# Performance work log

Measured on AMD Instinct MI355X. Metric: run time of the kernel, lower is better.

The kernel has to match this reference:

```python
import jax, jax.numpy as jnp
import numpy as np


def gcn_conv(x, edge_index, edge_weight, W, b):
    """PyG GCNConv: add self-loops (weight 1), symmetric degree norm, aggregate, linear."""
    N = x.shape[0]
    loop = jnp.arange(N, dtype=edge_index.dtype)
    src = jnp.concatenate([edge_index[0], loop])
    dst = jnp.concatenate([edge_index[1], loop])
    ew = jnp.concatenate([edge_weight, jnp.ones((N,), dtype=x.dtype)])
    deg = jax.ops.segment_sum(ew, dst, num_segments=N)
    dinv = jnp.where(deg > 0, jax.lax.rsqrt(deg), 0.0)
    norm = dinv[src] * ew * dinv[dst]            # [E+N]
    h = x @ W                                    # [N, out] transform first
    msg = h[src] * norm[:, None]                 # gather + scale
    out = jax.ops.segment_sum(msg, dst, num_segments=N)  # scatter-add
    return out + b


def l2norm(x, eps=1e-12):
    n = jnp.sqrt(jnp.sum(x * x, axis=-1, keepdims=True))
    return x / jnp.maximum(n, eps)


def setup_inputs() -> dict:
    key = jax.random.key(0)
    ks = jax.random.split(key, 16)
    N_net, E_net, N_dag, E_dag = 100000, 600000, 50000, 400000
    D_net, D_dag, H_net, H_dag = 128, 128, 128, 128
    s = lambda fan_in: 1.0 / np.sqrt(fan_in)
    return {
        "net_feat": jax.random.normal(ks[0], (N_net, D_net), jnp.float32),
        "net_edge_index": jax.random.randint(ks[1], (2, E_net), 0, N_net, jnp.int32),
        "net_edge_weights": jax.random.uniform(ks[2], (E_net,), jnp.float32),
        "dag_feat": jax.random.normal(ks[3], (N_dag, D_dag), jnp.float32),
        "dag_edge_index": jax.random.randint(ks[4], (2, E_dag), 0, N_dag, jnp.int32),
        "dag_edge_weights": jax.random.uniform(ks[5], (E_dag,), jnp.float32),
        "W_net": jax.random.normal(ks[6], (D_net, H_net), jnp.float32) * s(D_net),
        "b_net": jnp.zeros((H_net,), jnp.float32),
        "W_dag": jax.random.normal(ks[7], (D_dag, H_dag), jnp.float32) * s(D_dag),
        "b_dag": jnp.zeros((H_dag,), jnp.float32),
        "W1": jax.random.normal(ks[8], (H_net + H_dag, 64), jnp.float32) * s(H_net + H_dag),
        "b1": jnp.zeros((64,), jnp.float32),
        "W2": jax.random.normal(ks[9], (64, 1), jnp.float32) * s(64),
        "b2": jnp.zeros((1,), jnp.float32),
    }


def reference(net_feat, net_edge_index, net_edge_weights,
              dag_feat, dag_edge_index, dag_edge_weights,
              W_net, b_net, W_dag, b_dag, W1, b1, W2, b2):
    net_emb = jax.nn.relu(gcn_conv(net_feat, net_edge_index, net_edge_weights, W_net, b_net))
    dag_emb = jax.nn.relu(gcn_conv(dag_feat, dag_edge_index, dag_edge_weights, W_dag, b_dag))
    # normalize == True
    net_emb = l2norm(net_emb)
    dag_emb = l2norm(dag_emb)
    # net_batch/dag_batch are None: mean over nodes -> single state value
    net_vec = net_emb.mean(axis=0)
    dag_vec = dag_emb.mean(axis=0)
    combined = jnp.concatenate([net_vec, dag_vec], axis=-1)
    h = jax.nn.relu(combined @ W1 + b1)
    state_val = h @ W2 + b2
    return state_val
```

## Files before the change

### kernel.cpp

```cpp
#include <hip/hip_runtime.h>

#define FD 128
#define PAD 48
#define WSCALE 16777216.0f
#define WINV   5.9604645e-8f

typedef __attribute__((ext_vector_type(8))) short short8;
typedef __attribute__((ext_vector_type(4))) float f32x4;

__device__ inline unsigned short f2bf(float f) {
    unsigned u = __float_as_uint(f);
    return (unsigned short)((u + 0x7fffu + ((u >> 16) & 1u)) >> 16);
}
__device__ inline void bf4_to_f32(uint2 u, float& a, float& b, float& c, float& d) {
    a = __uint_as_float(u.x << 16);
    b = __uint_as_float(u.x & 0xffff0000u);
    c = __uint_as_float(u.y << 16);
    d = __uint_as_float(u.y & 0xffff0000u);
}
__device__ inline float pc_to_dinv(unsigned long long pv) {
    return rsqrtf((float)(pv & 0xffffffffull) * WINV + 1.0f);
}
__device__ inline void split1(float x, unsigned short& h, unsigned short& l) {
    unsigned u = __float_as_uint(x);
    unsigned hh = (u + 0x7fffu + ((u >> 16) & 1u)) >> 16;
    float r = x - __uint_as_float(hh << 16);
    unsigned u2 = __float_as_uint(r);
    h = (unsigned short)hh;
    l = (unsigned short)((u2 + 0x7fffu + ((u2 >> 16) & 1u)) >> 16);
}

__global__ __launch_bounds__(256) void bucket_pack(
        const int* __restrict__ ei_n, const float* __restrict__ ew_n,
        unsigned long long* __restrict__ pc_n, int2* __restrict__ el_n,
        int E_n, int GBn,
        const int* __restrict__ ei_d, const float* __restrict__ ew_d,
        unsigned long long* __restrict__ pc_d, int2* __restrict__ el_d,
        int E_d,
        const float* __restrict__ Wn, const float* __restrict__ Wd,
        unsigned short* __restrict__ Wpack) {
    int b = blockIdx.x;
    int packStart = (int)gridDim.x - 16;
    if (b >= packStart) {
        int p = b - packStart;
        int graph = p >> 3, pb = p & 7;
        const float* W = graph ? Wd : Wn;
        int c  = threadIdx.x & 127;
        int hh = threadIdx.x >> 7;
        int k0 = pb * 16 + hh * 8;
        short8 hv, lv;
        #pragma unroll
        for (int j = 0; j < 8; j++) {
            unsigned short hq, lq;
            split1(W[(k0 + j) * FD + c], hq, lq);
            hv[j] = (short)hq; lv[j] = (short)lq;
        }
        char* dst = (char*)Wpack + graph * 65536
                  + c * 256 + 16 * ((k0 >> 3) ^ (c & 15));
        *(short8*)dst = hv;
        *(short8*)(dst + 32768) = lv;
        return;
    }
    const int* ei; const float* ew; unsigned long long* pc; int2* el; int E, e;
    if (b < GBn) { ei = ei_n; ew = ew_n; pc = pc_n; el = el_n; E = E_n;
                   e = b * 256 + threadIdx.x; }
    else         { ei = ei_d; ew = ew_d; pc = pc_d; el = el_d; E = E_d;
                   e = (b - GBn) * 256 + threadIdx.x; }
    if (e < E) {
        int src = ei[e];
        int dst = ei[E + e];
        float w = ew[e];
        unsigned long long val =
            (1ull << 32) |
            (unsigned long long)(unsigned int)__float2uint_rn(w * WSCALE);
        unsigned long long old = atomicAdd(&pc[dst], val);
        unsigned int pos = (unsigned int)(old >> 32);
        if (pos < PAD)
            el[(size_t)dst * PAD + pos] = make_int2(src, __float_as_int(w));
    }
}

__global__ __launch_bounds__(256) void gemm_mfma(
        const float* __restrict__ X_n, const unsigned long long* __restrict__ pc_n,
        unsigned short* __restrict__ hs_n, int N_n, int Gn,
        const float* __restrict__ X_d, const unsigned long long* __restrict__ pc_d,
        unsigned short* __restrict__ hs_d, int N_d,
        const unsigned short* __restrict__ Wpack) {
    __shared__ unsigned short WL[2][128][128];

    const float* X; const unsigned long long* pc; unsigned short* hs; int N, r0;
    const char* wsrc;
    if (blockIdx.x < Gn) { X = X_n; pc = pc_n; hs = hs_n; N = N_n;
                           r0 = blockIdx.x * 128; wsrc = (const char*)Wpack; }
    else                 { X = X_d; pc = pc_d; hs = hs_d; N = N_d;
                           r0 = (blockIdx.x - Gn) * 128;
                           wsrc = (const char*)Wpack + 65536; }

    const int tid  = threadIdx.x;
    const int w    = tid >> 6;
    const int lane = tid & 63;
    const int c15  = lane & 15;
    const int g    = lane >> 4;

    {
        const float4* s4 = (const float4*)wsrc;
        float4* d4 = (float4*)WL;
        #pragma unroll
        for (int i = 0; i < 16; i++) d4[tid + i * 256] = s4[tid + i * 256];
    }
    __syncthreads();

    f32x4 acc[2][8] = {};

    const int row0 = r0 + 32 * w + c15;
    const float* x0p = X + (size_t)row0 * FD;
    const float* x1p = x0p + 16 * FD;
    const bool v0 = row0 < N, v1 = (row0 + 16) < N;

    #pragma unroll
    for (int kt = 0; kt < 4; kt++) {
        const int ko = 32 * kt + 8 * g;
        float4 a0 = {}, a1 = {}, c0 = {}, c1 = {};
        if (v0) { a0 = *(const float4*)(x0p + ko); c0 = *(const float4*)(x0p + ko + 4); }
        if (v1) { a1 = *(const float4*)(x1p + ko); c1 = *(const float4*)(x1p + ko + 4); }
        short8 ah0, al0, ah1, al1;
        {
            float xx[8] = {a0.x, a0.y, a0.z, a0.w, c0.x, c0.y, c0.z, c0.w};
            #pragma unroll
            for (int j = 0; j < 8; j++) {
                unsigned short hq, lq; split1(xx[j], hq, lq);
                ah0[j] = (short)hq; al0[j] = (short)lq;
            }
        }
        {
            float xx[8] = {a1.x, a1.y, a1.z, a1.w, c1.x, c1.y, c1.z, c1.w};
            #pragma unroll
            for (int j = 0; j < 8; j++) {
                unsigned short hq, lq; split1(xx[j], hq, lq);
                ah1[j] = (short)hq; al1[j] = (short)lq;
            }
        }

        const char* bbase = (const char*)WL + c15 * 256
                          + 16 * (((unsigned)(g + 4 * kt)) ^ (unsigned)c15);
        #pragma unroll
        for (int cf = 0; cf < 8; cf++) {
            short8 bh = *(const short8*)(bbase + cf * 4096);
            short8 bl = *(const short8*)(bbase + cf * 4096 + 32768);
            acc[0][cf] = __builtin_amdgcn_mfma_f32_16x16x32_bf16(ah0, bh, acc[0][cf], 0, 0, 0);
            acc[1][cf] = __builtin_amdgcn_mfma_f32_16x16x32_bf16(ah1, bh, acc[1][cf], 0, 0, 0);
            acc[0][cf] = __builtin_amdgcn_mfma_f32_16x16x32_bf16(al0, bh, acc[0][cf], 0, 0, 0);
            acc[1][cf] = __builtin_amdgcn_mfma_f32_16x16x32_bf16(al1, bh, acc[1][cf], 0, 0, 0);
            acc[0][cf] = __builtin_amdgcn_mfma_f32_16x16x32_bf16(ah0, bl, acc[0][cf], 0, 0, 0);
            acc[1][cf] = __builtin_amdgcn_mfma_f32_16x16x32_bf16(ah1, bl, acc[1][cf], 0, 0, 0);
        }
    }

    __syncthreads();
    unsigned short* OT = (unsigned short*)WL;
    #pragma unroll
    for (int rf = 0; rf < 2; rf++) {
        float dv[4];
        #pragma unroll
        for (int r = 0; r < 4; r++) {
            int row = r0 + 32 * w + 16 * rf + 4 * g + r;
            dv[r] = pc_to_dinv(row < N ? pc[row] : 0ull);
        }
        #pragma unroll
        for (int cf = 0; cf < 8; cf++) {
            #pragma unroll
            for (int r = 0; r < 4; r++) {
                int lrow = 32 * w + 16 * rf + 4 * g + r;
                unsigned byteo = (unsigned)(lrow * 256)
                               + (unsigned)((32 * cf + 2 * c15) ^ ((lrow & 15) << 4));
                *(unsigned short*)((char*)OT + byteo) = f2bf(acc[rf][cf][r] * dv[r]);
            }
        }
    }
    __syncthreads();
    #pragma unroll
    for (int p = 0; p < 8; p++) {
        int idx  = p * 256 + tid;
        int lrow = idx >> 4, ch = idx & 15;
        int row  = r0 + lrow;
        if (row < N) {
            uint4 v = *(const uint4*)((const char*)WL + lrow * 256
                                      + 16 * (ch ^ (lrow & 15)));
            *(uint4*)&hs[(size_t)row * FD + ch * 8] = v;
        }
    }
}

__global__ __launch_bounds__(256) void gather_reduce_both(
        const unsigned short* __restrict__ hs_n,
        const unsigned long long* __restrict__ pc_n, const int2* __restrict__ el_n,
        const float* __restrict__ b_n, int N_n,
        const unsigned short* __restrict__ hs_d,
        const unsigned long long* __restrict__ pc_d, const int2* __restrict__ el_d,
        const float* __restrict__ b_d, int N_d,
        float* __restrict__ vec) {
    __shared__ float accw[8][2 * FD];
    const int tid  = threadIdx.x;
    const int hw   = tid >> 5;
    const int sl   = tid & 31;

    float4 bbn = *(const float4*)&b_n[sl * 4];
    float4 bbd = *(const float4*)&b_d[sl * 4];
    float an0 = 0.f, an1 = 0.f, an2 = 0.f, an3 = 0.f;
    float ad0 = 0.f, ad1 = 0.f, ad2 = 0.f, ad3 = 0.f;

    const int total = N_n + N_d;
    const int stride = gridDim.x * 8;
    for (int t = blockIdx.x * 8 + hw; t < total; t += stride) {
        const bool isn = t < N_n;
        const int i = isn ? t : t - N_n;
        const unsigned short* hs = isn ? hs_n : hs_d;
        const unsigned long long* pc = isn ? pc_n : pc_d;
        const int2* el = (isn ? el_n : el_d) + (size_t)i * PAD;

        unsigned long long pv = pc[i];
        int cnt = (int)(pv >> 32);
        if (cnt > PAD) cnt = PAD;
        float dv = pc_to_dinv(pv);

        int2 my = (sl < cnt) ? el[sl] : make_int2(0, 0);

        float s0, s1, s2, s3;
        bf4_to_f32(*(const uint2*)&hs[(size_t)i * FD + sl * 4], s0, s1, s2, s3);
        float x0 = s0 * dv, x1 = s1 * dv, x2 = s2 * dv, x3 = s3 * dv;

        int lim = cnt < 32 ? cnt : 32;
        int j = 0;
        for (; j + 4 <= lim; j += 4) {
            int   q0 = __shfl(my.x, j,     32);
            float w0 = __int_as_float(__shfl(my.y, j,     32)) * dv;
            int   q1 = __shfl(my.x, j + 1, 32);
            float w1 = __int_as_float(__shfl(my.y, j + 1, 32)) * dv;
            int   q2 = __shfl(my.x, j + 2, 32);
            float w2 = __int_as_float(__shfl(my.y, j + 2, 32)) * dv;
            int   q3 = __shfl(my.x, j + 3, 32);
            float w3 = __int_as_float(__shfl(my.y, j + 3, 32)) * dv;
            uint2 u0 = *(const uint2*)&hs[(size_t)q0 * FD + sl * 4];
            uint2 u1 = *(const uint2*)&hs[(size_t)q1 * FD + sl * 4];
            uint2 u2 = *(const uint2*)&hs[(size_t)q2 * FD + sl * 4];
            uint2 u3 = *(const uint2*)&hs[(size_t)q3 * FD + sl * 4];
            float a, b2, c, d;
            bf4_to_f32(u0, a, b2, c, d);
            x0 = fmaf(a, w0, x0); x1 = fmaf(b2, w0, x1);
            x2 = fmaf(c, w0, x2); x3 = fmaf(d, w0, x3);
            bf4_to_f32(u1, a, b2, c, d);
            x0 = fmaf(a, w1, x0); x1 = fmaf(b2, w1, x1);
            x2 = fmaf(c, w1, x2); x3 = fmaf(d, w1, x3);
            bf4_to_f32(u2, a, b2, c, d);
            x0 = fmaf(a, w2, x0); x1 = fmaf(b2, w2, x1);
            x2 = fmaf(c, w2, x2); x3 = fmaf(d, w2, x3);
            bf4_to_f32(u3, a, b2, c, d);
            x0 = fmaf(a, w3, x0); x1 = fmaf(b2, w3, x1);
            x2 = fmaf(c, w3, x2); x3 = fmaf(d, w3, x3);
        }
        for (; j < lim; j++) {
            int   q = __shfl(my.x, j, 32);
            float w = __int_as_float(__shfl(my.y, j, 32)) * dv;
            uint2 u = *(const uint2*)&hs[(size_t)q * FD + sl * 4];
            float a, b2, c, d;
            bf4_to_f32(u, a, b2, c, d);
            x0 = fmaf(a, w, x0); x1 = fmaf(b2, w, x1);
            x2 = fmaf(c, w, x2); x3 = fmaf(d, w, x3);
        }
        for (; j < cnt; j++) {
            int2 p = el[j];
            float w = __int_as_float(p.y) * dv;
            uint2 u = *(const uint2*)&hs[(size_t)p.x * FD + sl * 4];
            float a, b2, c, d;
            bf4_to_f32(u, a, b2, c, d);
            x0 = fmaf(a, w, x0); x1 = fmaf(b2, w, x1);
            x2 = fmaf(c, w, x2); x3 = fmaf(d, w, x3);
        }

        float4 bb = isn ? bbn : bbd;
        x0 = fmaxf(x0 + bb.x, 0.f);
        x1 = fmaxf(x1 + bb.y, 0.f);
        x2 = fmaxf(x2 + bb.z, 0.f);
        x3 = fmaxf(x3 + bb.w, 0.f);
        float ss = fmaf(x0, x0, fmaf(x1, x1, fmaf(x2, x2, x3 * x3)));
        #pragma unroll
        for (int o = 16; o; o >>= 1) ss += __shfl_xor(ss, o);
        float inv = 1.0f / fmaxf(sqrtf(ss), 1e-12f);
        if (isn) {
            an0 = fmaf(x0, inv, an0); an1 = fmaf(x1, inv, an1);
            an2 = fmaf(x2, inv, an2); an3 = fmaf(x3, inv, an3);
        } else {
            ad0 = fmaf(x0, inv, ad0); ad1 = fmaf(x1, inv, ad1);
            ad2 = fmaf(x2, inv, ad2); ad3 = fmaf(x3, inv, ad3);
        }
    }
    accw[hw][sl * 4 + 0] = an0;
    accw[hw][sl * 4 + 1] = an1;
    accw[hw][sl * 4 + 2] = an2;
    accw[hw][sl * 4 + 3] = an3;
    accw[hw][FD + sl * 4 + 0] = ad0;
    accw[hw][FD + sl * 4 + 1] = ad1;
    accw[hw][FD + sl * 4 + 2] = ad2;
    accw[hw][FD + sl * 4 + 3] = ad3;
    __syncthreads();
    {
        float s = accw[0][tid] + accw[1][tid] + accw[2][tid] + accw[3][tid]
                + accw[4][tid] + accw[5][tid] + accw[6][tid] + accw[7][tid];
        unsafeAtomicAdd(&vec[tid], s);
    }
}

__global__ __launch_bounds__(256) void final_kernel(
        const float* __restrict__ vec,
        const float* __restrict__ W1, const float* __restrict__ b1,
        const float* __restrict__ W2, const float* __restrict__ b2,
        float* __restrict__ out, float invNnet, float invNdag) {
    __shared__ float part[4][64];
    int j = threadIdx.x & 63;
    int q = threadIdx.x >> 6;
    float h = 0.f;
    for (int k = q * 64; k < q * 64 + 64; k++) {
        float sc = (k < 128) ? invNnet : invNdag;
        h = fmaf(vec[k] * sc, W1[k * 64 + j], h);
    }
    part[q][j] = h;
    __syncthreads();
    if (threadIdx.x < 64) {
        float hh = b1[j] + part[0][j] + part[1][j] + part[2][j] + part[3][j];
        hh = fmaxf(hh, 0.f);
        float p = hh * W2[j];
        #pragma unroll
        for (int o = 32; o; o >>= 1) p += __shfl_xor(p, o);
        if (j == 0) out[0] = p + b2[0];
    }
}

extern "C" void kernel_launch(void* const* d_in, const int* in_sizes, int n_in,
                              void* d_out, int out_size, void* d_ws, size_t ws_size,
                              hipStream_t stream) {
    const float* net_feat = (const float*)d_in[0];
    const int*   net_ei   = (const int*)d_in[1];
    const float* net_ew   = (const float*)d_in[2];
    const float* dag_feat = (const float*)d_in[3];
    const int*   dag_ei   = (const int*)d_in[4];
    const float* dag_ew   = (const float*)d_in[5];
    const float* W_net    = (const float*)d_in[6];
    const float* b_net    = (const float*)d_in[7];
    const float* W_dag    = (const float*)d_in[8];
    const float* b_dag    = (const float*)d_in[9];
    const float* W1       = (const float*)d_in[10];
    const float* b1       = (const float*)d_in[11];
    const float* W2       = (const float*)d_in[12];
    const float* b2       = (const float*)d_in[13];

    const int N_net = in_sizes[0] / FD;
    const int E_net = in_sizes[2];
    const int N_dag = in_sizes[3] / FD;
    const int E_dag = in_sizes[5];
    const int GBn = (E_net + 255) / 256, GBd = (E_dag + 255) / 256;
    const int Gn  = (N_net + 127) / 128, Gd  = (N_dag + 127) / 128;

    char* w = (char*)d_ws;
    size_t o = 0;
    unsigned short* hs_net = (unsigned short*)(w + o); o += (size_t)2 * N_net * FD;
    unsigned short* hs_dag = (unsigned short*)(w + o); o += (size_t)2 * N_dag * FD;
    unsigned long long* pc_net = (unsigned long long*)(w + o); o += (size_t)8 * N_net;
    unsigned long long* pc_dag = (unsigned long long*)(w + o); o += (size_t)8 * N_dag;
    float* vec = (float*)(w + o); o += 256 * 4;
    size_t zbytes = (size_t)8 * (N_net + N_dag) + 256 * 4;
    int2* elist_net = (int2*)(w + o); o += (size_t)8 * N_net * PAD;
    int2* elist_dag = (int2*)(w + o); o += (size_t)8 * N_dag * PAD;
    unsigned short* Wpack = (unsigned short*)(w + o); o += 131072;

    hipMemsetAsync(pc_net, 0, zbytes, stream);

    bucket_pack<<<GBn + GBd + 16, 256, 0, stream>>>(
        net_ei, net_ew, pc_net, elist_net, E_net, GBn,
        dag_ei, dag_ew, pc_dag, elist_dag, E_dag,
        W_net, W_dag, Wpack);

    gemm_mfma<<<Gn + Gd, 256, 0, stream>>>(
        net_feat, pc_net, hs_net, N_net, Gn,
        dag_feat, pc_dag, hs_dag, N_dag, Wpack);

    gather_reduce_both<<<2048, 256, 0, stream>>>(
        hs_net, pc_net, elist_net, b_net, N_net,
        hs_dag, pc_dag, elist_dag, b_dag, N_dag, vec);

    final_kernel<<<1, 256, 0, stream>>>(vec, W1, b1, W2, b2, (float*)d_out,
                                        1.0f / (float)N_net, 1.0f / (float)N_dag);
}
```

Baseline: 346.7 us.

## Prefetch next node's metadata and batch neighbor gathers in groups of eight

After: 329.5 us. -5.0%, faster.

```diff
diff --git a/kernel.cpp b/kernel.cpp
--- a/kernel.cpp
+++ b/kernel.cpp
@@ -209,89 +209,139 @@
     float an0 = 0.f, an1 = 0.f, an2 = 0.f, an3 = 0.f;
     float ad0 = 0.f, ad1 = 0.f, ad2 = 0.f, ad3 = 0.f;
 
-    const int total = N_n + N_d;
+    const int total  = N_n + N_d;
     const int stride = gridDim.x * 8;
-    for (int t = blockIdx.x * 8 + hw; t < total; t += stride) {
-        const bool isn = t < N_n;
-        const int i = isn ? t : t - N_n;
-        const unsigned short* hs = isn ? hs_n : hs_d;
-        const unsigned long long* pc = isn ? pc_n : pc_d;
-        const int2* el = (isn ? el_n : el_d) + (size_t)i * PAD;
-
-        unsigned long long pv = pc[i];
-        int cnt = (int)(pv >> 32);
-        if (cnt > PAD) cnt = PAD;
-        float dv = pc_to_dinv(pv);
-
-        int2 my = (sl < cnt) ? el[sl] : make_int2(0, 0);
-
-        float s0, s1, s2, s3;
-        bf4_to_f32(*(const uint2*)&hs[(size_t)i * FD + sl * 4], s0, s1, s2, s3);
-        float x0 = s0 * dv, x1 = s1 * dv, x2 = s2 * dv, x3 = s3 * dv;
-
-        int lim = cnt < 32 ? cnt : 32;
-        int j = 0;
-        for (; j + 4 <= lim; j += 4) {
-            int   q0 = __shfl(my.x, j,     32);
-            float w0 = __int_as_float(__shfl(my.y, j,     32)) * dv;
-            int   q1 = __shfl(my.x, j + 1, 32);
-            float w1 = __int_as_float(__shfl(my.y, j + 1, 32)) * dv;
-            int   q2 = __shfl(my.x, j + 2, 32);
-            float w2 = __int_as_float(__shfl(my.y, j + 2, 32)) * dv;
-            int   q3 = __shfl(my.x, j + 3, 32);
-            float w3 = __int_as_float(__shfl(my.y, j + 3, 32)) * dv;
-            uint2 u0 = *(const uint2*)&hs[(size_t)q0 * FD + sl * 4];
-            uint2 u1 = *(const uint2*)&hs[(size_t)q1 * FD + sl * 4];
-            uint2 u2 = *(const uint2*)&hs[(size_t)q2 * FD + sl * 4];
-            uint2 u3 = *(const uint2*)&hs[(size_t)q3 * FD + sl * 4];
-            float a, b2, c, d;
-            bf4_to_f32(u0, a, b2, c, d);
-            x0 = fmaf(a, w0, x0); x1 = fmaf(b2, w0, x1);
-            x2 = fmaf(c, w0, x2); x3 = fmaf(d, w0, x3);
-            bf4_to_f32(u1, a, b2, c, d);
-            x0 = fmaf(a, w1, x0); x1 = fmaf(b2, w1, x1);
-            x2 = fmaf(c, w1, x2); x3 = fmaf(d, w1, x3);
-            bf4_to_f32(u2, a, b2, c, d);
-            x0 = fmaf(a, w2, x0); x1 = fmaf(b2, w2, x1);
-            x2 = fmaf(c, w2, x2); x3 = fmaf(d, w2, x3);
-            bf4_to_f32(u3, a, b2, c, d);
-            x0 = fmaf(a, w3, x0); x1 = fmaf(b2, w3, x1);
-            x2 = fmaf(c, w3, x2); x3 = fmaf(d, w3, x3);
-        }
-        for (; j < lim; j++) {
-            int   q = __shfl(my.x, j, 32);
-            float w = __int_as_float(__shfl(my.y, j, 32)) * dv;
-            uint2 u = *(const uint2*)&hs[(size_t)q * FD + sl * 4];
-            float a, b2, c, d;
-            bf4_to_f32(u, a, b2, c, d);
-            x0 = fmaf(a, w, x0); x1 = fmaf(b2, w, x1);
-            x2 = fmaf(c, w, x2); x3 = fmaf(d, w, x3);
-        }
-        for (; j < cnt; j++) {
-            int2 p = el[j];
-            float w = __int_as_float(p.y) * dv;
-            uint2 u = *(const uint2*)&hs[(size_t)p.x * FD + sl * 4];
-            float a, b2, c, d;
-            bf4_to_f32(u, a, b2, c, d);
-            x0 = fmaf(a, w, x0); x1 = fmaf(b2, w, x1);
-            x2 = fmaf(c, w, x2); x3 = fmaf(d, w, x3);
-        }
-
-        float4 bb = isn ? bbn : bbd;
-        x0 = fmaxf(x0 + bb.x, 0.f);
-        x1 = fmaxf(x1 + bb.y, 0.f);
-        x2 = fmaxf(x2 + bb.z, 0.f);
-        x3 = fmaxf(x3 + bb.w, 0.f);
-        float ss = fmaf(x0, x0, fmaf(x1, x1, fmaf(x2, x2, x3 * x3)));
-        #pragma unroll
-        for (int o = 16; o; o >>= 1) ss += __shfl_xor(ss, o);
-        float inv = 1.0f / fmaxf(sqrtf(ss), 1e-12f);
-        if (isn) {
-            an0 = fmaf(x0, inv, an0); an1 = fmaf(x1, inv, an1);
-            an2 = fmaf(x2, inv, an2); an3 = fmaf(x3, inv, an3);
-        } else {
-            ad0 = fmaf(x0, inv, ad0); ad1 = fmaf(x1, inv, ad1);
-            ad2 = fmaf(x2, inv, ad2); ad3 = fmaf(x3, inv, ad3);
+    int t0 = blockIdx.x * 8 + hw;
+
+    unsigned long long pvP = 0; int2 myP = make_int2(0, 0);
+    uint2 selfP = make_uint2(0u, 0u);
+
+    if (t0 < total) {
+        {
+            bool isn = t0 < N_n;
+            int i = isn ? t0 : t0 - N_n;
+            pvP   = (isn ? pc_n : pc_d)[i];
+            myP   = (isn ? el_n : el_d)[(size_t)i * PAD + sl];
+            selfP = *(const uint2*)&(isn ? hs_n : hs_d)[(size_t)i * FD + sl * 4];
+        }
+        for (int t = t0; t < total; t += stride) {
+            const unsigned long long pv = pvP;
+            const int2  my    = myP;
+            const uint2 selfu = selfP;
+            const bool isn = t < N_n;
+            const int  i   = isn ? t : t - N_n;
+            const unsigned short* hs = isn ? hs_n : hs_d;
+
+            int tn = t + stride;
+            if (tn < total) {
+                bool isn2 = tn < N_n;
+                int i2 = isn2 ? tn : tn - N_n;
+                pvP   = (isn2 ? pc_n : pc_d)[i2];
+                myP   = (isn2 ? el_n : el_d)[(size_t)i2 * PAD + sl];
+                selfP = *(const uint2*)&(isn2 ? hs_n : hs_d)[(size_t)i2 * FD + sl * 4];
+            }
+
+            int cnt = (int)(pv >> 32);
+            if (cnt > PAD) cnt = PAD;
+            const float dv = pc_to_dinv(pv);
+            const int lim = cnt < 32 ? cnt : 32;
+
+            float s0, s1, s2, s3;
+            bf4_to_f32(selfu, s0, s1, s2, s3);
+            float x0 = s0 * dv, x1 = s1 * dv, x2 = s2 * dv, x3 = s3 * dv;
+
+            uint2 ua[8]; float wa[8];
+            #pragma unroll
+            for (int u = 0; u < 8; u++) {
+                int   q  = __shfl(my.x, u, 32);
+                int   wi = __shfl(my.y, u, 32);
+                bool act = u < cnt;
+                wa[u] = act ? __int_as_float(wi) : 0.f;
+                int  qq = act ? q : i;
+                ua[u] = *(const uint2*)&hs[(size_t)qq * FD + sl * 4];
+            }
+            if (lim > 8) {
+                uint2 ub[8]; float wb[8];
+                #pragma unroll
+                for (int u = 0; u < 8; u++) {
+                    int  jj = 8 + u;
+                    int   q  = __shfl(my.x, jj, 32);
+                    int   wi = __shfl(my.y, jj, 32);
+                    bool act = jj < cnt;
+                    wb[u] = act ? __int_as_float(wi) : 0.f;
+                    int  qq = act ? q : i;
+                    ub[u] = *(const uint2*)&hs[(size_t)qq * FD + sl * 4];
+                }
+                #pragma unroll
+                for (int u = 0; u < 8; u++) {
+                    float w = wa[u] * dv;
+                    float a, b2, c, d; bf4_to_f32(ua[u], a, b2, c, d);
+                    x0 = fmaf(a, w, x0); x1 = fmaf(b2, w, x1);
+                    x2 = fmaf(c, w, x2); x3 = fmaf(d, w, x3);
+                }
+                #pragma unroll
+                for (int u = 0; u < 8; u++) {
+                    float w = wb[u] * dv;
+                    float a, b2, c, d; bf4_to_f32(ub[u], a, b2, c, d);
+                    x0 = fmaf(a, w, x0); x1 = fmaf(b2, w, x1);
+                    x2 = fmaf(c, w, x2); x3 = fmaf(d, w, x3);
+                }
+                for (int j = 16; j < lim; j += 8) {
+                    #pragma unroll
+                    for (int u = 0; u < 8; u++) {
+                        int  jj = j + u;
+                        int   q  = __shfl(my.x, jj & 31, 32);
+                        int   wi = __shfl(my.y, jj & 31, 32);
+                        bool act = jj < cnt;
+                        wa[u] = act ? __int_as_float(wi) : 0.f;
+                        int  qq = act ? q : i;
+                        ua[u] = *(const uint2*)&hs[(size_t)qq * FD + sl * 4];
+                    }
+                    #pragma unroll
+                    for (int u = 0; u < 8; u++) {
+                        float w = wa[u] * dv;
+                        float a, b2, c, d; bf4_to_f32(ua[u], a, b2, c, d);
+                        x0 = fmaf(a, w, x0); x1 = fmaf(b2, w, x1);
+                        x2 = fmaf(c, w, x2); x3 = fmaf(d, w, x3);
+                    }
+                }
+                if (cnt > 32) {
+                    const int2* el = (isn ? el_n : el_d) + (size_t)i * PAD;
+                    for (int j = 32; j < cnt; j++) {
+                        int2 p = el[j];
+                        float w = __int_as_float(p.y) * dv;
+                        uint2 u = *(const uint2*)&hs[(size_t)p.x * FD + sl * 4];
+                        float a, b2, c, d; bf4_to_f32(u, a, b2, c, d);
+                        x0 = fmaf(a, w, x0); x1 = fmaf(b2, w, x1);
+                        x2 = fmaf(c, w, x2); x3 = fmaf(d, w, x3);
+                    }
+                }
+            } else {
+                #pragma unroll
+                for (int u = 0; u < 8; u++) {
+                    float w = wa[u] * dv;
+                    float a, b2, c, d; bf4_to_f32(ua[u], a, b2, c, d);
+                    x0 = fmaf(a, w, x0); x1 = fmaf(b2, w, x1);
+                    x2 = fmaf(c, w, x2); x3 = fmaf(d, w, x3);
+                }
+            }
+
+            float4 bb = isn ? bbn : bbd;
+            x0 = fmaxf(x0 + bb.x, 0.f);
+            x1 = fmaxf(x1 + bb.y, 0.f);
+            x2 = fmaxf(x2 + bb.z, 0.f);
+            x3 = fmaxf(x3 + bb.w, 0.f);
+            float ss = fmaf(x0, x0, fmaf(x1, x1, fmaf(x2, x2, x3 * x3)));
+            #pragma unroll
+            for (int o = 16; o; o >>= 1) ss += __shfl_xor(ss, o);
+            float inv = 1.0f / fmaxf(sqrtf(ss), 1e-12f);
+            if (isn) {
+                an0 = fmaf(x0, inv, an0); an1 = fmaf(x1, inv, an1);
+                an2 = fmaf(x2, inv, an2); an3 = fmaf(x3, inv, an3);
+            } else {
+                ad0 = fmaf(x0, inv, ad0); ad1 = fmaf(x1, inv, ad1);
+                ad2 = fmaf(x2, inv, ad2); ad3 = fmaf(x3, inv, ad3);
+            }
         }
     }
     accw[hw][sl * 4 + 0] = an0;
```

## Software-pipeline neighbor gathers across nodes with fixed 12-slot prefetch

Applied to the files above, without the earlier changes.

After: 338.6 us. 1.02x faster.

```diff
diff --git a/kernel.cpp b/kernel.cpp
--- a/kernel.cpp
+++ b/kernel.cpp
@@ -210,71 +210,88 @@
     float ad0 = 0.f, ad1 = 0.f, ad2 = 0.f, ad3 = 0.f;
 
     const int total = N_n + N_d;
-    const int stride = gridDim.x * 8;
-    for (int t = blockIdx.x * 8 + hw; t < total; t += stride) {
+    const int S     = gridDim.x * 8;
+
+    struct GMeta {
+        unsigned long long pv;
+        int2 my;
+        uint2 self;
+        const unsigned short* hs;
+        const int2* el;
+        int i;
+    };
+
+    auto loadMeta = [&](int t, GMeta& m) {
         const bool isn = t < N_n;
         const int i = isn ? t : t - N_n;
-        const unsigned short* hs = isn ? hs_n : hs_d;
-        const unsigned long long* pc = isn ? pc_n : pc_d;
-        const int2* el = (isn ? el_n : el_d) + (size_t)i * PAD;
-
-        unsigned long long pv = pc[i];
-        int cnt = (int)(pv >> 32);
-        if (cnt > PAD) cnt = PAD;
-        float dv = pc_to_dinv(pv);
-
-        int2 my = (sl < cnt) ? el[sl] : make_int2(0, 0);
-
-        float s0, s1, s2, s3;
-        bf4_to_f32(*(const uint2*)&hs[(size_t)i * FD + sl * 4], s0, s1, s2, s3);
+        m.i  = i;
+        m.hs = isn ? hs_n : hs_d;
+        m.el = (isn ? el_n : el_d) + (size_t)i * PAD;
+        m.pv = (isn ? pc_n : pc_d)[i];
+        m.my = (sl < 16) ? m.el[sl] : make_int2(0, 0);
+        m.self = *(const uint2*)(m.hs + i * FD + sl * 4);
+    };
+
+    auto issueE = [&](const GMeta& m, uint2 (&e)[12]) {
+        int cn = (int)(m.pv >> 32); if (cn > PAD) cn = PAD;
+        #pragma unroll
+        for (int u = 0; u < 12; u++) {
+            int q  = __shfl(m.my.x, u, 32);
+            int qq = (u < cn) ? q : m.i;
+            e[u] = *(const uint2*)(m.hs + qq * FD + sl * 4);
+        }
+    };
+
+    auto PHASE = [&](GMeta& mc, GMeta& mn, uint2 (&ec)[12], uint2 (&en)[12],
+                     int t) {
+        const bool isn = t < N_n;
+        int cnt = (int)(mc.pv >> 32); if (cnt > PAD) cnt = PAD;
+        const float dv = pc_to_dinv(mc.pv);
+        const int2 mysv = mc.my;
+        const unsigned short* hs_c = mc.hs;
+        const int2* el_c = mc.el;
+        const int  i_c  = mc.i;
+        float s0, s1, s2, s3; bf4_to_f32(mc.self, s0, s1, s2, s3);
         float x0 = s0 * dv, x1 = s1 * dv, x2 = s2 * dv, x3 = s3 * dv;
 
-        int lim = cnt < 32 ? cnt : 32;
-        int j = 0;
-        for (; j + 4 <= lim; j += 4) {
-            int   q0 = __shfl(my.x, j,     32);
-            float w0 = __int_as_float(__shfl(my.y, j,     32)) * dv;
-            int   q1 = __shfl(my.x, j + 1, 32);
-            float w1 = __int_as_float(__shfl(my.y, j + 1, 32)) * dv;
-            int   q2 = __shfl(my.x, j + 2, 32);
-            float w2 = __int_as_float(__shfl(my.y, j + 2, 32)) * dv;
-            int   q3 = __shfl(my.x, j + 3, 32);
-            float w3 = __int_as_float(__shfl(my.y, j + 3, 32)) * dv;
-            uint2 u0 = *(const uint2*)&hs[(size_t)q0 * FD + sl * 4];
-            uint2 u1 = *(const uint2*)&hs[(size_t)q1 * FD + sl * 4];
-            uint2 u2 = *(const uint2*)&hs[(size_t)q2 * FD + sl * 4];
-            uint2 u3 = *(const uint2*)&hs[(size_t)q3 * FD + sl * 4];
-            float a, b2, c, d;
-            bf4_to_f32(u0, a, b2, c, d);
-            x0 = fmaf(a, w0, x0); x1 = fmaf(b2, w0, x1);
-            x2 = fmaf(c, w0, x2); x3 = fmaf(d, w0, x3);
-            bf4_to_f32(u1, a, b2, c, d);
-            x0 = fmaf(a, w1, x0); x1 = fmaf(b2, w1, x1);
-            x2 = fmaf(c, w1, x2); x3 = fmaf(d, w1, x3);
-            bf4_to_f32(u2, a, b2, c, d);
-            x0 = fmaf(a, w2, x0); x1 = fmaf(b2, w2, x1);
-            x2 = fmaf(c, w2, x2); x3 = fmaf(d, w2, x3);
-            bf4_to_f32(u3, a, b2, c, d);
-            x0 = fmaf(a, w3, x0); x1 = fmaf(b2, w3, x1);
-            x2 = fmaf(c, w3, x2); x3 = fmaf(d, w3, x3);
-        }
-        for (; j < lim; j++) {
-            int   q = __shfl(my.x, j, 32);
-            float w = __int_as_float(__shfl(my.y, j, 32)) * dv;
-            uint2 u = *(const uint2*)&hs[(size_t)q * FD + sl * 4];
-            float a, b2, c, d;
-            bf4_to_f32(u, a, b2, c, d);
+        { int t2 = t + 2 * S; loadMeta(t2 < total ? t2 : 0, mc); }
+
+        issueE(mn, en);
+
+        #pragma unroll
+        for (int u = 0; u < 12; u++) {
+            int wi = __shfl(mysv.y, u, 32);
+            float w = (u < cnt) ? __int_as_float(wi) * dv : 0.f;
+            float a, b2, c, d; bf4_to_f32(ec[u], a, b2, c, d);
             x0 = fmaf(a, w, x0); x1 = fmaf(b2, w, x1);
             x2 = fmaf(c, w, x2); x3 = fmaf(d, w, x3);
         }
-        for (; j < cnt; j++) {
-            int2 p = el[j];
-            float w = __int_as_float(p.y) * dv;
-            uint2 u = *(const uint2*)&hs[(size_t)p.x * FD + sl * 4];
-            float a, b2, c, d;
-            bf4_to_f32(u, a, b2, c, d);
-            x0 = fmaf(a, w, x0); x1 = fmaf(b2, w, x1);
-            x2 = fmaf(c, w, x2); x3 = fmaf(d, w, x3);
+        if (cnt > 12) {
+            uint2 et[4]; float wt[4];
+            #pragma unroll
+            for (int u = 0; u < 4; u++) {
+                int jj = 12 + u;
+                int q  = __shfl(mysv.x, jj, 32);
+                int wi = __shfl(mysv.y, jj, 32);
+                bool act = jj < cnt;
+                wt[u] = act ? __int_as_float(wi) * dv : 0.f;
+                int qq = act ? q : i_c;
+                et[u] = *(const uint2*)(hs_c + qq * FD + sl * 4);
+            }
+            #pragma unroll
+            for (int u = 0; u < 4; u++) {
+                float a, b2, c, d; bf4_to_f32(et[u], a, b2, c, d);
+                x0 = fmaf(a, wt[u], x0); x1 = fmaf(b2, wt[u], x1);
+                x2 = fmaf(c, wt[u], x2); x3 = fmaf(d, wt[u], x3);
+            }
+            for (int j = 16; j < cnt; j++) {
+                int2 p = el_c[j];
+                float w = __int_as_float(p.y) * dv;
+                uint2 u = *(const uint2*)(hs_c + p.x * FD + sl * 4);
+                float a, b2, c, d; bf4_to_f32(u, a, b2, c, d);
+                x0 = fmaf(a, w, x0); x1 = fmaf(b2, w, x1);
+                x2 = fmaf(c, w, x2); x3 = fmaf(d, w, x3);
+            }
         }
 
         float4 bb = isn ? bbn : bbd;
@@ -293,7 +310,23 @@
             ad0 = fmaf(x0, inv, ad0); ad1 = fmaf(x1, inv, ad1);
             ad2 = fmaf(x2, inv, ad2); ad3 = fmaf(x3, inv, ad3);
         }
-    }
+    };
+
+    int t = blockIdx.x * 8 + hw;
+    if (t < total) {
+        GMeta mA, mB;
+        uint2 e1[12], e2[12];
+        loadMeta(t, mA);
+        { int ts = t + S; loadMeta(ts < total ? ts : 0, mB); }
+        issueE(mA, e1);
+        while (true) {
+            PHASE(mA, mB, e1, e2, t);
+            t += S; if (t >= total) break;
+            PHASE(mB, mA, e2, e1, t);
+            t += S; if (t >= total) break;
+        }
+    }
+
     accw[hw][sl * 4 + 0] = an0;
     accw[hw][sl * 4 + 1] = an1;
     accw[hw][sl * 4 + 2] = an2;
```
